# Kernel optimization log

Measured on AMD Instinct MI355X. Metric: run time of the kernel, lower is better.

## Reference

```python
import jax, jax.numpy as jnp
import numpy as np

B, P, E, D, A = 128, 196, 2048, 512, 512


def setup_inputs() -> dict:
    key = jax.random.key(0)
    ks = jax.random.split(key, 8)
    s = lambda fan_in: 1.0 / np.sqrt(fan_in)
    return {
        "encoder_out": jax.random.normal(ks[0], (B, P, E), jnp.float32),
        "decoder_hidden": jax.random.normal(ks[1], (B, D), jnp.float32),
        "We": jax.random.uniform(ks[2], (E, A), jnp.float32, -s(E), s(E)),
        "be": jax.random.uniform(ks[3], (A,), jnp.float32, -s(E), s(E)),
        "Wd": jax.random.uniform(ks[4], (D, A), jnp.float32, -s(D), s(D)),
        "bd": jax.random.uniform(ks[5], (A,), jnp.float32, -s(D), s(D)),
        "Wf": jax.random.uniform(ks[6], (A, 1), jnp.float32, -s(A), s(A)),
        "bf": jax.random.uniform(ks[7], (1,), jnp.float32, -s(A), s(A)),
    }


def reference(encoder_out, decoder_hidden, We, be, Wd, bd, Wf, bf):
    # att1: [B, P, A]
    att1 = jnp.einsum("bpe,ea->bpa", encoder_out, We) + be
    # att2: [B, A]
    att2 = decoder_hidden @ Wd + bd
    # additive attention scores: [B, P]
    att = (jax.nn.relu(att1 + att2[:, None, :]) @ Wf + bf)[..., 0]
    alpha = jax.nn.softmax(att, axis=1)  # softmax over pixels
    # weighted sum over pixels: [B, E]
    awe = jnp.einsum("bpe,bp->be", encoder_out, alpha)
    return awe, alpha
```

## Files before the change

### kernel.cpp

```cpp
#include <hip/hip_runtime.h>
#include <hip/hip_bf16.h>

typedef __attribute__((ext_vector_type(4))) float f32x4;
typedef __attribute__((ext_vector_type(4))) unsigned int u32x4;
typedef __attribute__((ext_vector_type(8))) short s16x8;

#define B_  128
#define P_  196
#define E_  2048
#define D_  512
#define A_  512
#define M_  (B_*P_)

typedef __attribute__((address_space(1))) const unsigned int gu32;
typedef __attribute__((address_space(3))) unsigned int lu32;
__device__ __forceinline__ void gl_lds16(const void* g, void* l) {
  __builtin_amdgcn_global_load_lds((gu32*)g, (lu32*)l, 16, 0, 0);
}

#define WAIT_VM6() asm volatile("s_waitcnt vmcnt(6)" ::: "memory")
#define WAIT_VM0() asm volatile("s_waitcnt vmcnt(0)" ::: "memory")
#define WAIT_LGKM0() asm volatile("s_waitcnt lgkmcnt(0)" ::: "memory")

__global__ void we_conv_kernel(const float* __restrict__ We,
                               unsigned short* __restrict__ WeTs) {
  __shared__ float tile[32][33];
  const int tx = threadIdx.x, ty = threadIdx.y;
  const int a0 = blockIdx.x * 32, e0 = blockIdx.y * 32;
  tile[ty][tx] = We[(e0 + ty) * A_ + a0 + tx];
  __syncthreads();
  const float v = tile[tx][ty];
  const unsigned int u = __float_as_uint(v);
  const unsigned short r = (unsigned short)((u + 0x7fffu + ((u >> 16) & 1u)) >> 16);
  const int a = a0 + ty;
  const int kt = blockIdx.y;
  const int c8 = tx >> 3, j = tx & 7;
  const int dest = ((a * 32 + c8 * 8) ^ ((a & 7) << 3)) + j;
  WeTs[kt * 16384 + dest] = r;
}

__global__ void att2_kernel(const float* __restrict__ h, const float* __restrict__ Wd,
                            const float* __restrict__ bd, const float* __restrict__ be,
                            float* __restrict__ att2pb) {
  const int b = blockIdx.x;
  const int t = threadIdx.x;
  __shared__ float hs[D_];
  hs[t] = h[b * D_ + t];
  hs[t + 256] = h[b * D_ + t + 256];
  __syncthreads();
  float a0 = 0.f, a1 = 0.f;
  for (int d = 0; d < D_; ++d) {
    const float hv = hs[d];
    a0 = fmaf(hv, Wd[d * A_ + t], a0);
    a1 = fmaf(hv, Wd[d * A_ + t + 256], a1);
  }
  att2pb[b * A_ + t] = a0 + bd[t] + be[t];
  att2pb[b * A_ + t + 256] = a1 + bd[t + 256] + be[t + 256];
}

__device__ inline unsigned pk2(float a, float b) {
  union { __hip_bfloat162 h; unsigned u; } cv;
  cv.h = __float22bfloat162_rn(make_float2(a, b));
  return cv.u;
}
__device__ inline u32x4 cvt8(const f32x4 lo, const f32x4 hi) {
  u32x4 r;
  r[0] = pk2(lo[0], lo[1]);
  r[1] = pk2(lo[2], lo[3]);
  r[2] = pk2(hi[0], hi[1]);
  r[3] = pk2(hi[2], hi[3]);
  return r;
}

__launch_bounds__(512, 2)
__global__ void score_kernel(const float* __restrict__ enc,
                             const unsigned short* __restrict__ WeTs,
                             const float* __restrict__ att2pb,
                             const float* __restrict__ Wf,
                             float* __restrict__ att_part) {
  __shared__ unsigned short Bh[3][512 * 32];
  __shared__ unsigned short Ahs[3][128 * 32];

  const int bid = blockIdx.x;
  const int m0 = bid * 128;

  const int t = threadIdx.x;
  const int lane = t & 63, w = t >> 6;
  const int wm = (w >> 2) * 64;
  const int wn = (w & 3) * 128;

  const int ar = t >> 2, ac = t & 3;
  const float* aptr = enc + (size_t)(m0 + ar) * E_ + ac * 8;
  const int awz = (ar * 32 + ac * 8) ^ ((ar & 7) << 3);
  const int doff = t * 8;

  const int q = lane >> 4, fr = lane & 15;
  const int fx = (fr & 7) << 3;
  int fa[4], fb[8];
#pragma unroll
  for (int i = 0; i < 4; ++i) fa[i] = ((wm + i * 16 + fr) * 32 + q * 8) ^ fx;
#pragma unroll
  for (int j = 0; j < 8; ++j) fb[j] = ((wn + j * 16 + fr) * 32 + q * 8) ^ fx;

  const f32x4 zero = {0.f, 0.f, 0.f, 0.f};
  f32x4 acc[4][8];
#pragma unroll
  for (int mi = 0; mi < 4; ++mi)
#pragma unroll
    for (int ni = 0; ni < 8; ++ni) acc[mi][ni] = zero;

  unsigned short *bAc = &Ahs[0][0], *bA1 = &Ahs[1][0], *bA2 = &Ahs[2][0];
  unsigned short *bBc = &Bh[0][0],  *bB1 = &Bh[1][0],  *bB2 = &Bh[2][0];

  f32x4 aC0, aC1, aN0, aN1;

  {
    aC0 = *(const f32x4*)(aptr);
    aC1 = *(const f32x4*)(aptr + 4);
#pragma unroll
    for (int i = 0; i < 4; ++i)
      gl_lds16(WeTs + i * 4096 + doff, bBc + i * 4096 + doff);
    aN0 = *(const f32x4*)(aptr + 32);
    aN1 = *(const f32x4*)(aptr + 36);
#pragma unroll
    for (int i = 0; i < 4; ++i)
      gl_lds16(WeTs + 16384 + i * 4096 + doff, bB1 + i * 4096 + doff);
    const u32x4 av = cvt8(aC0, aC1);
    *(u32x4*)(bAc + awz) = av;
    aC0 = aN0; aC1 = aN1;
    WAIT_VM6();
    WAIT_LGKM0();
    __builtin_amdgcn_s_barrier();
  }

  for (int it = 0; it < 62; ++it) {
    const int kof = (it + 2) * 32;
    aN0 = *(const f32x4*)(aptr + kof);
    aN1 = *(const f32x4*)(aptr + kof + 4);
    const unsigned short* srcB = WeTs + (size_t)(it + 2) * 16384;
#pragma unroll
    for (int i = 0; i < 4; ++i)
      gl_lds16(srcB + i * 4096 + doff, bB2 + i * 4096 + doff);

    s16x8 fah[4], fbh[8];
#pragma unroll
    for (int j = 0; j < 8; ++j) fbh[j] = *(const s16x8*)(bBc + fb[j]);
#pragma unroll
    for (int i = 0; i < 4; ++i) fah[i] = *(const s16x8*)(bAc + fa[i]);
    __builtin_amdgcn_s_setprio(1);
#pragma unroll
    for (int mi = 0; mi < 4; ++mi)
#pragma unroll
      for (int ni = 0; ni < 8; ++ni)
        acc[mi][ni] = __builtin_amdgcn_mfma_f32_16x16x32_bf16(fah[mi], fbh[ni], acc[mi][ni], 0, 0, 0);
    __builtin_amdgcn_s_setprio(0);

    {
      const u32x4 av = cvt8(aC0, aC1);
      *(u32x4*)(bA1 + awz) = av;
    }
    aC0 = aN0; aC1 = aN1;

    WAIT_VM6();
    WAIT_LGKM0();
    __builtin_amdgcn_s_barrier();

    unsigned short* tmp;
    tmp = bAc; bAc = bA1; bA1 = bA2; bA2 = tmp;
    tmp = bBc; bBc = bB1; bB1 = bB2; bB2 = tmp;
  }

  {
    s16x8 fah[4], fbh[8];
#pragma unroll
    for (int j = 0; j < 8; ++j) fbh[j] = *(const s16x8*)(bBc + fb[j]);
#pragma unroll
    for (int i = 0; i < 4; ++i) fah[i] = *(const s16x8*)(bAc + fa[i]);
    __builtin_amdgcn_s_setprio(1);
#pragma unroll
    for (int mi = 0; mi < 4; ++mi)
#pragma unroll
      for (int ni = 0; ni < 8; ++ni)
        acc[mi][ni] = __builtin_amdgcn_mfma_f32_16x16x32_bf16(fah[mi], fbh[ni], acc[mi][ni], 0, 0, 0);
    __builtin_amdgcn_s_setprio(0);
    const u32x4 av = cvt8(aC0, aC1);
    *(u32x4*)(bA1 + awz) = av;
    WAIT_VM0();
    WAIT_LGKM0();
    __builtin_amdgcn_s_barrier();
  }

  {
    s16x8 fah[4], fbh[8];
#pragma unroll
    for (int j = 0; j < 8; ++j) fbh[j] = *(const s16x8*)(bB1 + fb[j]);
#pragma unroll
    for (int i = 0; i < 4; ++i) fah[i] = *(const s16x8*)(bA1 + fa[i]);
#pragma unroll
    for (int mi = 0; mi < 4; ++mi)
#pragma unroll
      for (int ni = 0; ni < 8; ++ni)
        acc[mi][ni] = __builtin_amdgcn_mfma_f32_16x16x32_bf16(fah[mi], fbh[ni], acc[mi][ni], 0, 0, 0);
  }

  const int colL = wn + fr;
  float wfv[8];
#pragma unroll
  for (int ni = 0; ni < 8; ++ni) wfv[ni] = Wf[colL + ni * 16];
#pragma unroll
  for (int mi = 0; mi < 4; ++mi) {
    const int rowb = m0 + wm + mi * 16 + (q << 2);
#pragma unroll
    for (int r = 0; r < 4; ++r) {
      const int row = rowb + r;
      const int bb = row / P_;
      const float* a2 = att2pb + bb * A_ + colL;
      float s = 0.f;
#pragma unroll
      for (int ni = 0; ni < 8; ++ni)
        s += fmaxf(acc[mi][ni][r] + a2[ni * 16], 0.f) * wfv[ni];
#pragma unroll
      for (int off = 1; off < 16; off <<= 1) s += __shfl_xor(s, off);
      if (fr == 0) att_part[row * 4 + (w & 3)] = s;
    }
  }
}

__global__ void softmax_awe_kernel(const float* __restrict__ enc,
                                   const float* __restrict__ att_part,
                                   float* __restrict__ out) {
  const int bid = blockIdx.x;
  const int b = bid >> 1, ch = bid & 1;
  const int t = threadIdx.x;
  __shared__ float sm[256];
  __shared__ float alpha_s[P_];

  float av = -1e30f;
  if (t < P_) {
    const float* apt = att_part + (b * P_ + t) * 4;
    av = (apt[0] + apt[1]) + (apt[2] + apt[3]);
  }
  sm[t] = av;
  __syncthreads();
  for (int st = 128; st > 0; st >>= 1) {
    if (t < st) sm[t] = fmaxf(sm[t], sm[t + st]);
    __syncthreads();
  }
  const float mx = sm[0];
  __syncthreads();
  float ev = 0.f;
  if (t < P_) ev = __expf(av - mx);
  sm[t] = ev;
  __syncthreads();
  for (int st = 128; st > 0; st >>= 1) {
    if (t < st) sm[t] += sm[t + st];
    __syncthreads();
  }
  const float denom = sm[0];
  const float al = ev / denom;
  if (t < P_) {
    alpha_s[t] = al;
    if (ch == 0) out[B_ * E_ + b * P_ + t] = al;
  }
  __syncthreads();

  const int e0 = ch * 1024 + t * 4;
  const float* ebase = enc + (size_t)b * P_ * E_ + e0;
  f32x4 acc = {0.f, 0.f, 0.f, 0.f};
  for (int p = 0; p < P_; ++p) {
    const f32x4 v = *(const f32x4*)(ebase + (size_t)p * E_);
    const float a = alpha_s[p];
    acc.x += a * v.x; acc.y += a * v.y; acc.z += a * v.z; acc.w += a * v.w;
  }
  *(f32x4*)(out + b * E_ + e0) = acc;
}

extern "C" void kernel_launch(void* const* d_in, const int* in_sizes, int n_in,
                              void* d_out, int out_size, void* d_ws, size_t ws_size,
                              hipStream_t stream) {
  const float* enc = (const float*)d_in[0];
  const float* h   = (const float*)d_in[1];
  const float* We  = (const float*)d_in[2];
  const float* be  = (const float*)d_in[3];
  const float* Wd  = (const float*)d_in[4];
  const float* bd  = (const float*)d_in[5];
  const float* Wf  = (const float*)d_in[6];
  float* out = (float*)d_out;

  float* att2pb = (float*)d_ws;
  float* att_part = att2pb + B_ * A_;
  unsigned short* WeTs = (unsigned short*)(att_part + M_ * 4);

  we_conv_kernel<<<dim3(A_ / 32, E_ / 32), dim3(32, 32), 0, stream>>>(We, WeTs);
  att2_kernel<<<B_, 256, 0, stream>>>(h, Wd, bd, be, att2pb);
  score_kernel<<<M_ / 128, 512, 0, stream>>>(enc, WeTs, att2pb, Wf, att_part);
  softmax_awe_kernel<<<B_ * 2, 256, 0, stream>>>(enc, att_part, out);
}
```

Before: 133.7 us.

## Double score-kernel threads to 1024 with smaller per-wave tiles and split B fragment loads

The score GEMM block grows from 512 to 1024 threads while keeping the same 128x512 block tile. Each wave now computes a 32x128 sub-tile instead of 64x128, and each thread stages 4 encoder floats per k-step instead of 8. B fragments are loaded from LDS in two halves, interleaved with MFMAs, to reduce register pressure, and the vmcnt wait is adjusted to match the fewer loads per thread. The aim is more resident waves per CU to hide memory and LDS latency. The cost is more LDS fragment reads per MFMA, since B tiles are now re-read by twice as many waves.

```diff
diff --git a/kernel.cpp b/kernel.cpp
--- a/kernel.cpp
+++ b/kernel.cpp
@@ -1,6 +1,7 @@
 #include <hip/hip_runtime.h>
 #include <hip/hip_bf16.h>
 
+typedef __attribute__((ext_vector_type(2))) unsigned int u32x2;
 typedef __attribute__((ext_vector_type(4))) float f32x4;
 typedef __attribute__((ext_vector_type(4))) unsigned int u32x4;
 typedef __attribute__((ext_vector_type(8))) short s16x8;
@@ -18,7 +19,7 @@
   __builtin_amdgcn_global_load_lds((gu32*)g, (lu32*)l, 16, 0, 0);
 }
 
-#define WAIT_VM6() asm volatile("s_waitcnt vmcnt(6)" ::: "memory")
+#define WAIT_VM3() asm volatile("s_waitcnt vmcnt(3)" ::: "memory")
 #define WAIT_VM0() asm volatile("s_waitcnt vmcnt(0)" ::: "memory")
 #define WAIT_LGKM0() asm volatile("s_waitcnt lgkmcnt(0)" ::: "memory")
 
@@ -63,16 +64,8 @@
   cv.h = __float22bfloat162_rn(make_float2(a, b));
   return cv.u;
 }
-__device__ inline u32x4 cvt8(const f32x4 lo, const f32x4 hi) {
-  u32x4 r;
-  r[0] = pk2(lo[0], lo[1]);
-  r[1] = pk2(lo[2], lo[3]);
-  r[2] = pk2(hi[0], hi[1]);
-  r[3] = pk2(hi[2], hi[3]);
-  return r;
-}
-
-__launch_bounds__(512, 2)
+
+__launch_bounds__(1024, 4)
 __global__ void score_kernel(const float* __restrict__ enc,
                              const unsigned short* __restrict__ WeTs,
                              const float* __restrict__ att2pb,
@@ -86,82 +79,86 @@
 
   const int t = threadIdx.x;
   const int lane = t & 63, w = t >> 6;
-  const int wm = (w >> 2) * 64;
+  const int wm = (w >> 2) * 32;
   const int wn = (w & 3) * 128;
 
-  const int ar = t >> 2, ac = t & 3;
-  const float* aptr = enc + (size_t)(m0 + ar) * E_ + ac * 8;
-  const int awz = (ar * 32 + ac * 8) ^ ((ar & 7) << 3);
+  const int ar = t >> 3, ac4 = t & 7;
+  const float* aptr = enc + (size_t)(m0 + ar) * E_ + ac4 * 4;
+  const int awz = (ar * 32 + ac4 * 4) ^ ((ar & 7) << 3);
+
   const int doff = t * 8;
 
   const int q = lane >> 4, fr = lane & 15;
   const int fx = (fr & 7) << 3;
-  int fa[4], fb[8];
-#pragma unroll
-  for (int i = 0; i < 4; ++i) fa[i] = ((wm + i * 16 + fr) * 32 + q * 8) ^ fx;
+  int fa[2], fb[8];
+#pragma unroll
+  for (int i = 0; i < 2; ++i) fa[i] = ((wm + i * 16 + fr) * 32 + q * 8) ^ fx;
 #pragma unroll
   for (int j = 0; j < 8; ++j) fb[j] = ((wn + j * 16 + fr) * 32 + q * 8) ^ fx;
 
   const f32x4 zero = {0.f, 0.f, 0.f, 0.f};
-  f32x4 acc[4][8];
-#pragma unroll
-  for (int mi = 0; mi < 4; ++mi)
+  f32x4 acc[2][8];
+#pragma unroll
+  for (int mi = 0; mi < 2; ++mi)
 #pragma unroll
     for (int ni = 0; ni < 8; ++ni) acc[mi][ni] = zero;
 
   unsigned short *bAc = &Ahs[0][0], *bA1 = &Ahs[1][0], *bA2 = &Ahs[2][0];
   unsigned short *bBc = &Bh[0][0],  *bB1 = &Bh[1][0],  *bB2 = &Bh[2][0];
 
-  f32x4 aC0, aC1, aN0, aN1;
+  f32x4 aC, aN;
 
   {
-    aC0 = *(const f32x4*)(aptr);
-    aC1 = *(const f32x4*)(aptr + 4);
-#pragma unroll
-    for (int i = 0; i < 4; ++i)
-      gl_lds16(WeTs + i * 4096 + doff, bBc + i * 4096 + doff);
-    aN0 = *(const f32x4*)(aptr + 32);
-    aN1 = *(const f32x4*)(aptr + 36);
-#pragma unroll
-    for (int i = 0; i < 4; ++i)
-      gl_lds16(WeTs + 16384 + i * 4096 + doff, bB1 + i * 4096 + doff);
-    const u32x4 av = cvt8(aC0, aC1);
-    *(u32x4*)(bAc + awz) = av;
-    aC0 = aN0; aC1 = aN1;
-    WAIT_VM6();
+    aC = *(const f32x4*)(aptr);
+    gl_lds16(WeTs + doff, bBc + doff);
+    gl_lds16(WeTs + 8192 + doff, bBc + 8192 + doff);
+    aN = *(const f32x4*)(aptr + 32);
+    gl_lds16(WeTs + 16384 + doff, bB1 + doff);
+    gl_lds16(WeTs + 16384 + 8192 + doff, bB1 + 8192 + doff);
+    u32x2 av; av[0] = pk2(aC[0], aC[1]); av[1] = pk2(aC[2], aC[3]);
+    *(u32x2*)(bAc + awz) = av;
+    aC = aN;
+    WAIT_VM3();
     WAIT_LGKM0();
     __builtin_amdgcn_s_barrier();
   }
 
   for (int it = 0; it < 62; ++it) {
     const int kof = (it + 2) * 32;
-    aN0 = *(const f32x4*)(aptr + kof);
-    aN1 = *(const f32x4*)(aptr + kof + 4);
-    const unsigned short* srcB = WeTs + (size_t)(it + 2) * 16384;
-#pragma unroll
-    for (int i = 0; i < 4; ++i)
-      gl_lds16(srcB + i * 4096 + doff, bB2 + i * 4096 + doff);
-
-    s16x8 fah[4], fbh[8];
-#pragma unroll
-    for (int j = 0; j < 8; ++j) fbh[j] = *(const s16x8*)(bBc + fb[j]);
-#pragma unroll
-    for (int i = 0; i < 4; ++i) fah[i] = *(const s16x8*)(bAc + fa[i]);
+    aN = *(const f32x4*)(aptr + kof);
+    const unsigned short* sb = WeTs + (size_t)(it + 2) * 16384;
+    gl_lds16(sb + doff, bB2 + doff);
+    gl_lds16(sb + 8192 + doff, bB2 + 8192 + doff);
+
+    s16x8 fah[2], fbh[4];
+    fah[0] = *(const s16x8*)(bAc + fa[0]);
+    fah[1] = *(const s16x8*)(bAc + fa[1]);
+#pragma unroll
+    for (int j = 0; j < 4; ++j) fbh[j] = *(const s16x8*)(bBc + fb[j]);
     __builtin_amdgcn_s_setprio(1);
 #pragma unroll
-    for (int mi = 0; mi < 4; ++mi)
-#pragma unroll
-      for (int ni = 0; ni < 8; ++ni)
+    for (int mi = 0; mi < 2; ++mi)
+#pragma unroll
+      for (int ni = 0; ni < 4; ++ni)
         acc[mi][ni] = __builtin_amdgcn_mfma_f32_16x16x32_bf16(fah[mi], fbh[ni], acc[mi][ni], 0, 0, 0);
     __builtin_amdgcn_s_setprio(0);
+#pragma unroll
+    for (int j = 0; j < 4; ++j) fbh[j] = *(const s16x8*)(bBc + fb[4 + j]);
+    __builtin_amdgcn_s_setprio(1);
+#pragma unroll
+    for (int mi = 0; mi < 2; ++mi)
+#pragma unroll
+      for (int ni = 0; ni < 4; ++ni)
+        acc[mi][4 + ni] = __builtin_amdgcn_mfma_f32_16x16x32_bf16(fah[mi], fbh[ni], acc[mi][4 + ni], 0, 0, 0);
+    __builtin_amdgcn_s_setprio(0);
 
     {
-      const u32x4 av = cvt8(aC0, aC1);
-      *(u32x4*)(bA1 + awz) = av;
+      u32x2 av; av[0] = pk2(aC[0], aC[1]); av[1] = pk2(aC[2], aC[3]);
+      *(u32x2*)(bA1 + awz) = av;
     }
-    aC0 = aN0; aC1 = aN1;
-
-    WAIT_VM6();
+    aC = aN;
+
+    WAIT_VM3();
     WAIT_LGKM0();
     __builtin_amdgcn_s_barrier();
 
@@ -171,36 +168,48 @@
   }
 
   {
-    s16x8 fah[4], fbh[8];
-#pragma unroll
-    for (int j = 0; j < 8; ++j) fbh[j] = *(const s16x8*)(bBc + fb[j]);
-#pragma unroll
-    for (int i = 0; i < 4; ++i) fah[i] = *(const s16x8*)(bAc + fa[i]);
-    __builtin_amdgcn_s_setprio(1);
-#pragma unroll
-    for (int mi = 0; mi < 4; ++mi)
-#pragma unroll
-      for (int ni = 0; ni < 8; ++ni)
+    s16x8 fah[2], fbh[4];
+    fah[0] = *(const s16x8*)(bAc + fa[0]);
+    fah[1] = *(const s16x8*)(bAc + fa[1]);
+#pragma unroll
+    for (int j = 0; j < 4; ++j) fbh[j] = *(const s16x8*)(bBc + fb[j]);
+#pragma unroll
+    for (int mi = 0; mi < 2; ++mi)
+#pragma unroll
+      for (int ni = 0; ni < 4; ++ni)
         acc[mi][ni] = __builtin_amdgcn_mfma_f32_16x16x32_bf16(fah[mi], fbh[ni], acc[mi][ni], 0, 0, 0);
-    __builtin_amdgcn_s_setprio(0);
-    const u32x4 av = cvt8(aC0, aC1);
-    *(u32x4*)(bA1 + awz) = av;
+#pragma unroll
+    for (int j = 0; j < 4; ++j) fbh[j] = *(const s16x8*)(bBc + fb[4 + j]);
+#pragma unroll
+    for (int mi = 0; mi < 2; ++mi)
+#pragma unroll
+      for (int ni = 0; ni < 4; ++ni)
+        acc[mi][4 + ni] = __builtin_amdgcn_mfma_f32_16x16x32_bf16(fah[mi], fbh[ni], acc[mi][4 + ni], 0, 0, 0);
+    u32x2 av; av[0] = pk2(aC[0], aC[1]); av[1] = pk2(aC[2], aC[3]);
+    *(u32x2*)(bA1 + awz) = av;
     WAIT_VM0();
     WAIT_LGKM0();
     __builtin_amdgcn_s_barrier();
   }
 
   {
-    s16x8 fah[4], fbh[8];
-#pragma unroll
-    for (int j = 0; j < 8; ++j) fbh[j] = *(const s16x8*)(bB1 + fb[j]);
-#pragma unroll
-    for (int i = 0; i < 4; ++i) fah[i] = *(const s16x8*)(bA1 + fa[i]);
-#pragma unroll
-    for (int mi = 0; mi < 4; ++mi)
-#pragma unroll
-      for (int ni = 0; ni < 8; ++ni)
+    s16x8 fah[2], fbh[4];
+    fah[0] = *(const s16x8*)(bA1 + fa[0]);
+    fah[1] = *(const s16x8*)(bA1 + fa[1]);
+#pragma unroll
+    for (int j = 0; j < 4; ++j) fbh[j] = *(const s16x8*)(bB1 + fb[j]);
+#pragma unroll
+    for (int mi = 0; mi < 2; ++mi)
+#pragma unroll
+      for (int ni = 0; ni < 4; ++ni)
         acc[mi][ni] = __builtin_amdgcn_mfma_f32_16x16x32_bf16(fah[mi], fbh[ni], acc[mi][ni], 0, 0, 0);
+#pragma unroll
+    for (int j = 0; j < 4; ++j) fbh[j] = *(const s16x8*)(bB1 + fb[4 + j]);
+#pragma unroll
+    for (int mi = 0; mi < 2; ++mi)
+#pragma unroll
+      for (int ni = 0; ni < 4; ++ni)
+        acc[mi][4 + ni] = __builtin_amdgcn_mfma_f32_16x16x32_bf16(fah[mi], fbh[ni], acc[mi][4 + ni], 0, 0, 0);
   }
 
   const int colL = wn + fr;
@@ -208,7 +217,7 @@
 #pragma unroll
   for (int ni = 0; ni < 8; ++ni) wfv[ni] = Wf[colL + ni * 16];
 #pragma unroll
-  for (int mi = 0; mi < 4; ++mi) {
+  for (int mi = 0; mi < 2; ++mi) {
     const int rowb = m0 + wm + mi * 16 + (q << 2);
 #pragma unroll
     for (int r = 0; r < 4; ++r) {
@@ -293,6 +302,6 @@
 
   we_conv_kernel<<<dim3(A_ / 32, E_ / 32), dim3(32, 32), 0, stream>>>(We, WeTs);
   att2_kernel<<<B_, 256, 0, stream>>>(h, Wd, bd, be, att2pb);
-  score_kernel<<<M_ / 128, 512, 0, stream>>>(enc, WeTs, att2pb, Wf, att_part);
+  score_kernel<<<M_ / 128, 1024, 0, stream>>>(enc, WeTs, att2pb, Wf, att_part);
   softmax_awe_kernel<<<B_ * 2, 256, 0, stream>>>(enc, att_part, out);
 }
```

New measurement: 130.3 us, median of 2. -2.5%, faster.
